# Kernel tuning notes

Hardware: AMD Instinct MI355X
Metric: run time of the kernel (lower is better)

## Reference

```python
import jax, jax.numpy as jnp
import numpy as np

N_NODES = 50000
N_EDGES = 600000
N_GRAPHS = 64


def _linear_init(key, fan_in, fan_out):
    # torch nn.Linear default: U(-1/sqrt(fan_in), 1/sqrt(fan_in))
    s = 1.0 / np.sqrt(fan_in)
    kw, kb = jax.random.split(key)
    W = jax.random.uniform(kw, (fan_in, fan_out), jnp.float32, -s, s)
    b = jax.random.uniform(kb, (fan_out,), jnp.float32, -s, s)
    return W, b


def setup_inputs() -> dict:
    key = jax.random.key(0)
    ks = jax.random.split(key, 7)
    x = jax.random.normal(ks[0], (N_NODES, 128), jnp.float32)
    edge_index = jax.random.randint(ks[1], (2, N_EDGES), 0, N_NODES, dtype=jnp.int32).astype(jnp.int64)
    batch = jnp.sort(jax.random.randint(ks[2], (N_NODES,), 0, N_GRAPHS, dtype=jnp.int32)).astype(jnp.int64)
    W1, b1 = _linear_init(ks[3], 128, 256)
    W2, b2 = _linear_init(ks[4], 256, 256)
    W3, b3 = _linear_init(ks[5], 256, 128)
    W4, b4 = _linear_init(ks[6], 128, 10)
    return dict(x=x, edge_index=edge_index, batch=batch,
                W1=W1, b1=b1, W2=W2, b2=b2, W3=W3, b3=b3, W4=W4, b4=b4)


def _gcn_conv(h, src, dst, W, b, n_nodes):
    # PyG GCNConv: add self-loops (src/dst already include them),
    # symmetric normalization D^{-1/2} (A+I) D^{-1/2} h W + b.
    h = h @ W                                      # [N, Cout]
    deg = jax.ops.segment_sum(jnp.ones(src.shape[0], h.dtype), dst, num_segments=n_nodes)
    dinv = jnp.where(deg > 0, jax.lax.rsqrt(deg), 0.0)
    norm = dinv[src] * dinv[dst]                   # [E+N]
    msg = h[src] * norm[:, None]                   # gather + scale per edge
    agg = jax.ops.segment_sum(msg, dst, num_segments=n_nodes)  # scatter-add
    return agg + b


def reference(x, edge_index, batch, W1, b1, W2, b2, W3, b3, W4, b4):
    n = x.shape[0]
    loops = jnp.arange(n, dtype=edge_index.dtype)
    src = jnp.concatenate([edge_index[0], loops])
    dst = jnp.concatenate([edge_index[1], loops])
    # GCNBlock (activate_last=True since dense layers follow)
    h = jax.nn.relu(_gcn_conv(x, src, dst, W1, b1, n))
    h = jax.nn.relu(_gcn_conv(h, src, dst, W2, b2, n))
    # global_mean_pool over batch segments
    sums = jax.ops.segment_sum(h, batch, num_segments=N_GRAPHS)          # [G, 256]
    counts = jax.ops.segment_sum(jnp.ones((n,), h.dtype), batch, num_segments=N_GRAPHS)
    g = sums / jnp.maximum(counts, 1.0)[:, None]
    # DenseBlock [256 -> 128 -> 10], activate_last=False
    g = jax.nn.relu(g @ W3 + b3)
    return g @ W4 + b4
```

## Files before the change

### kernel.cpp

```cpp
#include <hip/hip_runtime.h>

typedef unsigned short u16;
typedef unsigned int u32;
typedef __attribute__((ext_vector_type(8))) short s16x8;
typedef __attribute__((ext_vector_type(4))) float f32x4;

#define NN 50000
#define NE 600000
#define NG 64

__device__ __forceinline__ u16 f2bf(float f) {
    u32 u = __float_as_uint(f);
    u32 r = (u + 0x7fffu + ((u >> 16) & 1u)) >> 16;
    return (u16)r;
}
__device__ __forceinline__ float bf2f(u16 h) {
    return __uint_as_float(((u32)h) << 16);
}
__device__ __forceinline__ void gll16(const void* g, void* l) {
    __builtin_amdgcn_global_load_lds((const __attribute__((address_space(1))) u32*)g,
                                     (__attribute__((address_space(3))) u32*)l, 16, 0, 0);
}

__global__ void k_hist(const int* __restrict__ dst, int* __restrict__ cnt, int ne) {
    int e = blockIdx.x * blockDim.x + threadIdx.x;
    if (e < ne) atomicAdd(&cnt[dst[e]], 1);
}

__global__ __launch_bounds__(256)
void k_scan1(const int* __restrict__ cnt, int* __restrict__ bsum, int n) {
    int i = blockIdx.x * 256 + threadIdx.x;
    int v = (i < n) ? cnt[i] : 0;
#pragma unroll
    for (int off = 32; off > 0; off >>= 1) v += __shfl_down(v, off, 64);
    __shared__ int ws[4];
    int lane = threadIdx.x & 63, w = threadIdx.x >> 6;
    if (lane == 0) ws[w] = v;
    __syncthreads();
    if (threadIdx.x == 0) bsum[blockIdx.x] = ws[0] + ws[1] + ws[2] + ws[3];
}

__global__ __launch_bounds__(256)
void k_scan2(int* __restrict__ bsum, int nb) {
    int t = threadIdx.x;
    int v = (t < nb) ? bsum[t] : 0;
    int lane = t & 63, w = t >> 6;
    int inc = v;
#pragma unroll
    for (int off = 1; off < 64; off <<= 1) {
        int x = __shfl_up(inc, off, 64);
        if (lane >= off) inc += x;
    }
    __shared__ int wtot[4];
    if (lane == 63) wtot[w] = inc;
    __syncthreads();
    int wo = 0;
    for (int j = 0; j < w; ++j) wo += wtot[j];
    if (t < nb) bsum[t] = wo + inc - v;
}

__global__ __launch_bounds__(256)
void k_scan3(const int* __restrict__ cnt, const int* __restrict__ boff,
             int* __restrict__ rowptr, int* __restrict__ cursor,
             float* __restrict__ dinv, int n) {
    int i = blockIdx.x * 256 + threadIdx.x;
    int v = (i < n) ? cnt[i] : 0;
    int lane = threadIdx.x & 63, w = threadIdx.x >> 6;
    int inc = v;
#pragma unroll
    for (int off = 1; off < 64; off <<= 1) {
        int x = __shfl_up(inc, off, 64);
        if (lane >= off) inc += x;
    }
    __shared__ int wtot[4];
    if (lane == 63) wtot[w] = inc;
    __syncthreads();
    int wo = boff[blockIdx.x];
    for (int j = 0; j < w; ++j) wo += wtot[j];
    if (i < n) {
        int excl = wo + inc - v;
        rowptr[i] = excl;
        cursor[i] = excl;
        dinv[i] = rsqrtf(1.0f + (float)v);
        if (i == n - 1) rowptr[n] = excl + v;
    }
}

__global__ void k_fill(const int* __restrict__ src, const int* __restrict__ dst,
                       int* __restrict__ cursor, int* __restrict__ csr_src, int ne) {
    int e = blockIdx.x * blockDim.x + threadIdx.x;
    if (e < ne) {
        int pos = atomicAdd(&cursor[dst[e]], 1);
        csr_src[pos] = src[e];
    }
}

__device__ __forceinline__ void wsplit_tiled(const float* __restrict__ W,
                                             u16* __restrict__ hi, u16* __restrict__ lo,
                                             int gid) {
    int n = gid & 255, kgrp = gid >> 8;
    int kbase = kgrp * 8;
#pragma unroll
    for (int j = 0; j < 8; ++j) {
        float w = W[(size_t)(kbase + j) * 256 + n];
        u16 h = f2bf(w);
        hi[(size_t)gid * 8 + j] = h;
        lo[(size_t)gid * 8 + j] = f2bf(w - bf2f(h));
    }
}

__global__ __launch_bounds__(256)
void k_preamble(const float* __restrict__ x, u16* __restrict__ xbf,
                const float* __restrict__ W1, u16* __restrict__ w1hi, u16* __restrict__ w1lo,
                const float* __restrict__ W2, u16* __restrict__ w2hi, u16* __restrict__ w2lo,
                float* __restrict__ sums, int* __restrict__ cnt,
                const int* __restrict__ batch, float* __restrict__ counts) {
    const int XB = (NN * 32 + 255) / 256;
    const int CB = (NN + 255) / 256;
    int b = blockIdx.x, t = threadIdx.x;
    if (b < XB) {
        int i = b * 256 + t;
        if (i < NN * 32) {
            float4 v = ((const float4*)x)[i];
            ushort4 o;
            o.x = f2bf(v.x); o.y = f2bf(v.y); o.z = f2bf(v.z); o.w = f2bf(v.w);
            ((ushort4*)xbf)[i] = o;
        }
        return;
    }
    b -= XB;
    if (b < 16) { wsplit_tiled(W1, w1hi, w1lo, b * 256 + t); return; }
    b -= 16;
    if (b < 32) { wsplit_tiled(W2, w2hi, w2lo, b * 256 + t); return; }
    b -= 32;
    if (b < 64) { sums[b * 256 + t] = 0.f; return; }
    b -= 64;
    if (b < CB) {
        int i = b * 256 + t;
        if (i < NN) cnt[i] = 0;
        return;
    }
    b -= CB;
    if (b == 0) {
        __shared__ int lb[65];
        if (t <= 64) {
            int lo = 0, hi = NN;
            while (lo < hi) {
                int mid = (lo + hi) >> 1;
                if (batch[mid] < t) lo = mid + 1; else hi = mid;
            }
            lb[t] = lo;
        }
        __syncthreads();
        if (t < 64) counts[t] = (float)(lb[t + 1] - lb[t]);
    }
}

__device__ __forceinline__ void fma8(float* a, const uint4& v, float w) {
    a[0] += bf2f((u16)v.x) * w; a[1] += bf2f((u16)(v.x >> 16)) * w;
    a[2] += bf2f((u16)v.y) * w; a[3] += bf2f((u16)(v.y >> 16)) * w;
    a[4] += bf2f((u16)v.z) * w; a[5] += bf2f((u16)(v.z >> 16)) * w;
    a[6] += bf2f((u16)v.w) * w; a[7] += bf2f((u16)(v.w >> 16)) * w;
}
__device__ __forceinline__ void fma4(float* a, const uint2& v, float w) {
    a[0] += bf2f((u16)v.x) * w; a[1] += bf2f((u16)(v.x >> 16)) * w;
    a[2] += bf2f((u16)v.y) * w; a[3] += bf2f((u16)(v.y >> 16)) * w;
}

template<int C>
__global__ __launch_bounds__(256)
void k_agg_gather(const int* __restrict__ rowptr, const int* __restrict__ csr_src,
                  const float* __restrict__ dinv, const u16* __restrict__ hb,
                  u16* __restrict__ out, int n) {
    constexpr int VL = C / 32;
    int tid = threadIdx.x;
    int node = (blockIdx.x * 256 + tid) >> 5;
    if (node >= n) return;
    int sl = tid & 31;
    int hbase = tid & 32;
    int beg = rowptr[node], end = rowptr[node + 1];
    int m = end - beg;
    float di = dinv[node];
    float a0[VL], a1[VL];
    if constexpr (VL == 8) {
        uint4 v = ((const uint4*)hb)[(size_t)node * 32 + sl];
#pragma unroll
        for (int i = 0; i < 8; ++i) a1[i] = 0.f;
        a0[0] = bf2f((u16)v.x) * di; a0[1] = bf2f((u16)(v.x >> 16)) * di;
        a0[2] = bf2f((u16)v.y) * di; a0[3] = bf2f((u16)(v.y >> 16)) * di;
        a0[4] = bf2f((u16)v.z) * di; a0[5] = bf2f((u16)(v.z >> 16)) * di;
        a0[6] = bf2f((u16)v.w) * di; a0[7] = bf2f((u16)(v.w >> 16)) * di;
    } else {
        uint2 v = ((const uint2*)hb)[(size_t)node * 32 + sl];
#pragma unroll
        for (int i = 0; i < 4; ++i) a1[i] = 0.f;
        a0[0] = bf2f((u16)v.x) * di; a0[1] = bf2f((u16)(v.x >> 16)) * di;
        a0[2] = bf2f((u16)v.y) * di; a0[3] = bf2f((u16)(v.y >> 16)) * di;
    }
    for (int base = 0; base < m; base += 32) {
        int c = m - base; if (c > 32) c = 32;
        int sid = 0; float w = 0.f;
        if (sl < c) { sid = csr_src[beg + base + sl]; w = dinv[sid]; }
        int cr = (c + 3) & ~3;
        for (int e = 0; e < cr; e += 4) {
            int   s0 = __shfl(sid, hbase + e, 64),     s1 = __shfl(sid, hbase + e + 1, 64);
            int   s2 = __shfl(sid, hbase + e + 2, 64), s3 = __shfl(sid, hbase + e + 3, 64);
            float w0 = __shfl(w, hbase + e, 64),       w1 = __shfl(w, hbase + e + 1, 64);
            float w2 = __shfl(w, hbase + e + 2, 64),   w3 = __shfl(w, hbase + e + 3, 64);
            if constexpr (VL == 8) {
                uint4 r0 = ((const uint4*)hb)[(size_t)s0 * 32 + sl];
                uint4 r1 = ((const uint4*)hb)[(size_t)s1 * 32 + sl];
                uint4 r2 = ((const uint4*)hb)[(size_t)s2 * 32 + sl];
                uint4 r3 = ((const uint4*)hb)[(size_t)s3 * 32 + sl];
                fma8(a0, r0, w0); fma8(a1, r1, w1); fma8(a0, r2, w2); fma8(a1, r3, w3);
            } else {
                uint2 r0 = ((const uint2*)hb)[(size_t)s0 * 32 + sl];
                uint2 r1 = ((const uint2*)hb)[(size_t)s1 * 32 + sl];
                uint2 r2 = ((const uint2*)hb)[(size_t)s2 * 32 + sl];
                uint2 r3 = ((const uint2*)hb)[(size_t)s3 * 32 + sl];
                fma4(a0, r0, w0); fma4(a1, r1, w1); fma4(a0, r2, w2); fma4(a1, r3, w3);
            }
        }
    }
    if constexpr (VL == 8) {
        uint4 o;
        o.x = (u32)f2bf((a0[0] + a1[0]) * di) | ((u32)f2bf((a0[1] + a1[1]) * di) << 16);
        o.y = (u32)f2bf((a0[2] + a1[2]) * di) | ((u32)f2bf((a0[3] + a1[3]) * di) << 16);
        o.z = (u32)f2bf((a0[4] + a1[4]) * di) | ((u32)f2bf((a0[5] + a1[5]) * di) << 16);
        o.w = (u32)f2bf((a0[6] + a1[6]) * di) | ((u32)f2bf((a0[7] + a1[7]) * di) << 16);
        ((uint4*)out)[(size_t)node * 32 + sl] = o;
    } else {
        uint2 o;
        o.x = (u32)f2bf((a0[0] + a1[0]) * di) | ((u32)f2bf((a0[1] + a1[1]) * di) << 16);
        o.y = (u32)f2bf((a0[2] + a1[2]) * di) | ((u32)f2bf((a0[3] + a1[3]) * di) << 16);
        ((uint2*)out)[(size_t)node * 32 + sl] = o;
    }
}

template<bool POOL>
__global__ __launch_bounds__(512, 4)
void k_gemm_mfma(const u16* __restrict__ A, const u16* __restrict__ Bhi,
                 const u16* __restrict__ Blo,
                 const float* __restrict__ bias, u16* __restrict__ out_bf,
                 const int* __restrict__ batch, float* __restrict__ pool,
                 int M, int K) {
    __shared__ u16 ldsA[2][4096];
    const int tid = threadIdx.x, lane = tid & 63, wid = tid >> 6;
    const int bm = blockIdx.x * 128;
    const int wr = (wid >> 2) * 64, wc = (wid & 3) * 64;
    const int lr = lane & 15, kg = lane >> 4;

    const int srow = wid * 16 + (lane >> 2);
    const int sslot = lane & 3;
    const int ssw = (srow ^ (srow >> 2)) & 3;
    int srg = bm + srow; if (srg >= M) srg = M - 1;
    const u16* sbase = A + (size_t)srg * K + ((sslot ^ ssw) << 3);

    f32x4 acc[4][4];
#pragma unroll
    for (int i = 0; i < 4; ++i)
#pragma unroll
        for (int j = 0; j < 4; ++j) acc[i][j] = (f32x4){0.f, 0.f, 0.f, 0.f};

    const int nt = K >> 5;
    gll16(sbase, &ldsA[0][wid * 512]);
    __syncthreads();

    for (int t = 0; t < nt; ++t) {
        int cur = t & 1;
        if (t + 1 < nt)
            gll16(sbase + ((t + 1) << 5), &ldsA[cur ^ 1][wid * 512]);

        s16x8 bh[4], bl[4];
#pragma unroll
        for (int fn = 0; fn < 4; ++fn) {
            size_t off = ((size_t)((t << 2) + kg) * 256 + wc + fn * 16 + lr) * 8;
            bh[fn] = *(const s16x8*)&Bhi[off];
            bl[fn] = *(const s16x8*)&Blo[off];
        }
        const u16* lb = ldsA[cur];
        s16x8 a[4];
#pragma unroll
        for (int fm = 0; fm < 4; ++fm) {
            int r = wr + fm * 16 + lr;
            a[fm] = *(const s16x8*)&lb[r * 32 + ((kg ^ ((r ^ (r >> 2)) & 3)) << 3)];
        }
#pragma unroll
        for (int fn = 0; fn < 4; ++fn)
#pragma unroll
            for (int fm = 0; fm < 4; ++fm) {
                acc[fm][fn] = __builtin_amdgcn_mfma_f32_16x16x32_bf16(a[fm], bh[fn], acc[fm][fn], 0, 0, 0);
                acc[fm][fn] = __builtin_amdgcn_mfma_f32_16x16x32_bf16(a[fm], bl[fn], acc[fm][fn], 0, 0, 0);
            }
        __syncthreads();
    }

#pragma unroll
    for (int fn = 0; fn < 4; ++fn) {
        int col = wc + fn * 16 + lr;
        float bv = bias[col];
        if (!POOL) {
#pragma unroll
            for (int fm = 0; fm < 4; ++fm) {
                int rbase = bm + wr + fm * 16 + kg * 4;
#pragma unroll
                for (int r = 0; r < 4; ++r) {
                    int row = rbase + r;
                    if (row < M)
                        out_bf[(size_t)row * 256 + col] = f2bf(fmaxf(acc[fm][fn][r] + bv, 0.f));
                }
            }
        } else {
            int gcur = -1;
            float run = 0.f;
#pragma unroll
            for (int fm = 0; fm < 4; ++fm) {
                int rbase = bm + wr + fm * 16 + kg * 4;
#pragma unroll
                for (int r = 0; r < 4; ++r) {
                    int row = rbase + r;
                    if (row < M) {
                        int g = batch[row];
                        float v = fmaxf(acc[fm][fn][r] + bv, 0.f);
                        if (g != gcur) {
                            if (gcur >= 0) atomicAdd(&pool[gcur * 256 + col], run);
                            gcur = g;
                            run = 0.f;
                        }
                        run += v;
                    }
                }
            }
            if (gcur >= 0) atomicAdd(&pool[gcur * 256 + col], run);
        }
    }
}

__global__ __launch_bounds__(128)
void k_dense(const float* __restrict__ sums, const float* __restrict__ counts,
             const float* __restrict__ W3, const float* __restrict__ b3,
             const float* __restrict__ W4, const float* __restrict__ b4,
             float* __restrict__ out) {
    __shared__ float g[256];
    __shared__ float hid[128];
    int gi = blockIdx.x;
    int t = threadIdx.x;
    float inv = 1.0f / fmaxf(counts[gi], 1.0f);
    for (int c = t; c < 256; c += 128) g[c] = sums[gi * 256 + c] * inv;
    __syncthreads();
    float acc = b3[t];
    for (int k = 0; k < 256; ++k) acc += g[k] * W3[k * 128 + t];
    hid[t] = fmaxf(acc, 0.0f);
    __syncthreads();
    if (t < 10) {
        float o = b4[t];
        for (int k = 0; k < 128; ++k) o += hid[k] * W4[k * 10 + t];
        out[gi * 10 + t] = o;
    }
}

extern "C" void kernel_launch(void* const* d_in, const int* in_sizes, int n_in,
                              void* d_out, int out_size, void* d_ws, size_t ws_size,
                              hipStream_t stream) {
    const float* x   = (const float*)d_in[0];
    const int*  eidx = (const int*)d_in[1];
    const int*  batch= (const int*)d_in[2];
    const float* W1 = (const float*)d_in[3];
    const float* b1 = (const float*)d_in[4];
    const float* W2 = (const float*)d_in[5];
    const float* b2 = (const float*)d_in[6];
    const float* W3 = (const float*)d_in[7];
    const float* b3 = (const float*)d_in[8];
    const float* W4 = (const float*)d_in[9];
    const float* b4 = (const float*)d_in[10];
    float* out = (float*)d_out;

    const int N = NN, E = NE, G = NG;
    const int* src = eidx;
    const int* dst = eidx + E;
    const int NB = (N + 255) / 256;

    char* p = (char*)d_ws;
    auto alloc = [&](size_t bytes) { char* r = p; p += (bytes + 255) & ~(size_t)255; return r; };
    u16*   h1bf   = (u16*)alloc((size_t)N * 256 * 2);
    u16*   xbf    = (u16*)alloc((size_t)N * 128 * 2);
    float* dinv   = (float*)alloc((size_t)N * 4);
    float* sums   = (float*)alloc((size_t)G * 256 * 4);
    float* counts = (float*)alloc((size_t)G * 4);
    int*   cnt    = (int*)alloc((size_t)N * 4);
    int*   rowptr = (int*)alloc((size_t)(N + 1) * 4);
    int*   bsum   = (int*)alloc((size_t)NB * 4);
    int*   csr    = (int*)alloc((size_t)E * 4);
    u16*   agg1   = (u16*)alloc((size_t)N * 128 * 2);
    u16*   agg2   = (u16*)alloc((size_t)N * 256 * 2);
    u16*   w1hi   = (u16*)alloc((size_t)256 * 128 * 2);
    u16*   w1lo   = (u16*)alloc((size_t)256 * 128 * 2);
    u16*   w2hi   = (u16*)alloc((size_t)256 * 256 * 2);
    u16*   w2lo   = (u16*)alloc((size_t)256 * 256 * 2);
    int*   cursor = cnt;

    const int XB = (NN * 32 + 255) / 256;
    const int CB = (NN + 255) / 256;
    int pre_blocks = XB + 16 + 32 + 64 + CB + 1;
    k_preamble<<<pre_blocks, 256, 0, stream>>>(x, xbf, W1, w1hi, w1lo, W2, w2hi, w2lo,
                                               sums, cnt, batch, counts);

    k_hist<<<(E + 255) / 256, 256, 0, stream>>>(dst, cnt, E);
    k_scan1<<<NB, 256, 0, stream>>>(cnt, bsum, N);
    k_scan2<<<1, 256, 0, stream>>>(bsum, NB);
    k_scan3<<<NB, 256, 0, stream>>>(cnt, bsum, rowptr, cursor, dinv, N);
    k_fill<<<(E + 255) / 256, 256, 0, stream>>>(src, dst, cursor, csr, E);

    k_agg_gather<128><<<(N + 7) / 8, 256, 0, stream>>>(rowptr, csr, dinv, xbf, agg1, N);
    int gblocks = (N + 127) / 128;
    k_gemm_mfma<false><<<gblocks, 512, 0, stream>>>(agg1, w1hi, w1lo, b1, h1bf,
                                                    nullptr, nullptr, N, 128);

    k_agg_gather<256><<<(N + 7) / 8, 256, 0, stream>>>(rowptr, csr, dinv, h1bf, agg2, N);
    k_gemm_mfma<true><<<gblocks, 512, 0, stream>>>(agg2, w2hi, w2lo, b2, nullptr,
                                                   batch, sums, N, 256);

    k_dense<<<G, 128, 0, stream>>>(sums, counts, W3, b3, W4, b4, out);
}
```

Baseline: 221.2 us.

## Replace LDS double-buffered GEMM with register-direct MFMA GEMM using 64-row tiles

The node GEMMs used a 128x256 tile with 512 threads, staging A through LDS via global_load_lds double buffering and a barrier every k-step. They now use a 64-row tile with 4 waves, each covering 64 columns. Every wave loads its A fragments straight from global memory into registers, and the K loop is fully unrolled by a template parameter. This removes the LDS traffic and barriers and doubles the number of blocks. In exchange, all four waves load the same A rows redundantly, which relies on L1/L2 reuse, and B is re-read across twice as many blocks.

Result: slower. 243.0 us (+9.8%).

```diff
diff --git a/kernel.cpp b/kernel.cpp
--- a/kernel.cpp
+++ b/kernel.cpp
@@ -16,10 +16,6 @@
 }
 __device__ __forceinline__ float bf2f(u16 h) {
     return __uint_as_float(((u32)h) << 16);
-}
-__device__ __forceinline__ void gll16(const void* g, void* l) {
-    __builtin_amdgcn_global_load_lds((const __attribute__((address_space(1))) u32*)g,
-                                     (__attribute__((address_space(3))) u32*)l, 16, 0, 0);
 }
 
 __global__ void k_hist(const int* __restrict__ dst, int* __restrict__ cnt, int ne) {
@@ -237,24 +233,27 @@
     }
 }
 
-template<bool POOL>
-__global__ __launch_bounds__(512, 4)
-void k_gemm_mfma(const u16* __restrict__ A, const u16* __restrict__ Bhi,
-                 const u16* __restrict__ Blo,
-                 const float* __restrict__ bias, u16* __restrict__ out_bf,
-                 const int* __restrict__ batch, float* __restrict__ pool,
-                 int M, int K) {
-    __shared__ u16 ldsA[2][4096];
-    const int tid = threadIdx.x, lane = tid & 63, wid = tid >> 6;
-    const int bm = blockIdx.x * 128;
-    const int wr = (wid >> 2) * 64, wc = (wid & 3) * 64;
+template<bool POOL, int KK>
+__global__ __launch_bounds__(256)
+void k_gemm_reg(const u16* __restrict__ A, const u16* __restrict__ Bhi,
+                const u16* __restrict__ Blo,
+                const float* __restrict__ bias, u16* __restrict__ out_bf,
+                const int* __restrict__ batch, float* __restrict__ pool,
+                int M) {
+    const int lane = threadIdx.x & 63, wid = threadIdx.x >> 6;
+    const int bm = blockIdx.x * 64;
+    const int wc = wid * 64;
     const int lr = lane & 15, kg = lane >> 4;
 
-    const int srow = wid * 16 + (lane >> 2);
-    const int sslot = lane & 3;
-    const int ssw = (srow ^ (srow >> 2)) & 3;
-    int srg = bm + srow; if (srg >= M) srg = M - 1;
-    const u16* sbase = A + (size_t)srg * K + ((sslot ^ ssw) << 3);
+    const u16* arow[4];
+#pragma unroll
+    for (int fm = 0; fm < 4; ++fm) {
+        int row = bm + fm * 16 + lr;
+        if (row >= M) row = M - 1;
+        arow[fm] = A + (size_t)row * KK + kg * 8;
+    }
+    const u16* bh_p = Bhi + ((u32)kg * 256 + wc + lr) * 8;
+    const u16* bl_p = Blo + ((u32)kg * 256 + wc + lr) * 8;
 
     f32x4 acc[4][4];
 #pragma unroll
@@ -262,28 +261,17 @@
 #pragma unroll
         for (int j = 0; j < 4; ++j) acc[i][j] = (f32x4){0.f, 0.f, 0.f, 0.f};
 
-    const int nt = K >> 5;
-    gll16(sbase, &ldsA[0][wid * 512]);
-    __syncthreads();
-
-    for (int t = 0; t < nt; ++t) {
-        int cur = t & 1;
-        if (t + 1 < nt)
-            gll16(sbase + ((t + 1) << 5), &ldsA[cur ^ 1][wid * 512]);
-
-        s16x8 bh[4], bl[4];
+#pragma unroll
+    for (int t = 0; t < KK / 32; ++t) {
+        s16x8 a[4], bh[4], bl[4];
+#pragma unroll
+        for (int fm = 0; fm < 4; ++fm)
+            a[fm] = *(const s16x8*)(arow[fm] + t * 32);
 #pragma unroll
         for (int fn = 0; fn < 4; ++fn) {
-            size_t off = ((size_t)((t << 2) + kg) * 256 + wc + fn * 16 + lr) * 8;
-            bh[fn] = *(const s16x8*)&Bhi[off];
-            bl[fn] = *(const s16x8*)&Blo[off];
-        }
-        const u16* lb = ldsA[cur];
-        s16x8 a[4];
-#pragma unroll
-        for (int fm = 0; fm < 4; ++fm) {
-            int r = wr + fm * 16 + lr;
-            a[fm] = *(const s16x8*)&lb[r * 32 + ((kg ^ ((r ^ (r >> 2)) & 3)) << 3)];
+            u32 off = (u32)t * 8192 + (u32)fn * 128;
+            bh[fn] = *(const s16x8*)&bh_p[off];
+            bl[fn] = *(const s16x8*)&bl_p[off];
         }
 #pragma unroll
         for (int fn = 0; fn < 4; ++fn)
@@ -292,7 +280,6 @@
                 acc[fm][fn] = __builtin_amdgcn_mfma_f32_16x16x32_bf16(a[fm], bh[fn], acc[fm][fn], 0, 0, 0);
                 acc[fm][fn] = __builtin_amdgcn_mfma_f32_16x16x32_bf16(a[fm], bl[fn], acc[fm][fn], 0, 0, 0);
             }
-        __syncthreads();
     }
 
 #pragma unroll
@@ -302,7 +289,7 @@
         if (!POOL) {
 #pragma unroll
             for (int fm = 0; fm < 4; ++fm) {
-                int rbase = bm + wr + fm * 16 + kg * 4;
+                int rbase = bm + fm * 16 + kg * 4;
 #pragma unroll
                 for (int r = 0; r < 4; ++r) {
                     int row = rbase + r;
@@ -315,7 +302,7 @@
             float run = 0.f;
 #pragma unroll
             for (int fm = 0; fm < 4; ++fm) {
-                int rbase = bm + wr + fm * 16 + kg * 4;
+                int rbase = bm + fm * 16 + kg * 4;
 #pragma unroll
                 for (int r = 0; r < 4; ++r) {
                     int row = rbase + r;
@@ -412,13 +399,13 @@
     k_fill<<<(E + 255) / 256, 256, 0, stream>>>(src, dst, cursor, csr, E);
 
     k_agg_gather<128><<<(N + 7) / 8, 256, 0, stream>>>(rowptr, csr, dinv, xbf, agg1, N);
-    int gblocks = (N + 127) / 128;
-    k_gemm_mfma<false><<<gblocks, 512, 0, stream>>>(agg1, w1hi, w1lo, b1, h1bf,
-                                                    nullptr, nullptr, N, 128);
+    int gblocks = (N + 63) / 64;
+    k_gemm_reg<false, 128><<<gblocks, 256, 0, stream>>>(agg1, w1hi, w1lo, b1, h1bf,
+                                                        nullptr, nullptr, N);
 
     k_agg_gather<256><<<(N + 7) / 8, 256, 0, stream>>>(rowptr, csr, dinv, h1bf, agg2, N);
-    k_gemm_mfma<true><<<gblocks, 512, 0, stream>>>(agg2, w2hi, w2lo, b2, nullptr,
-                                                   batch, sums, N, 256);
+    k_gemm_reg<true, 256><<<gblocks, 256, 0, stream>>>(agg2, w2hi, w2lo, b2, nullptr,
+                                                       batch, sums, N);
 
     k_dense<<<G, 128, 0, stream>>>(sums, counts, W3, b3, W4, b4, out);
 }
```
